# Kernel tuning notes

Measured on AMD Instinct MI355X. Metric: run time of the kernel, lower is better.

Reference implementation:

```python
import jax, jax.numpy as jnp
import numpy as np
import math

B, SQ, SK, HEADS, DH = 4, 4096, 308, 8, 64
INNER = HEADS * DH


def setup_inputs() -> dict:
    key = jax.random.key(0)
    k1, k2, k3, k4, k5 = jax.random.split(key, 5)
    q = jax.random.normal(k1, (B, SQ, INNER), dtype=jnp.float32)
    k = jax.random.normal(k2, (B, SK, INNER), dtype=jnp.float32)
    v = jax.random.normal(k3, (B, SK, INNER), dtype=jnp.float32)
    # mask_scale: positive multiplicative rescale (H*W / mask_area in original)
    mask_scale = jax.random.uniform(k4, (B, HEADS, SQ, SK), dtype=jnp.float32) + 0.5
    # mask_bool: region membership mask (masks > 0.5 in original)
    mask_bool = jax.random.randint(k5, (B, HEADS, SQ, SK), 0, 2) > 0
    return {"q": q, "k": k, "v": v, "mask_scale": mask_scale,
            "mask_bool": mask_bool, "heads": HEADS}


def reference(q, k, v, mask_scale, mask_bool, heads):
    b, sq, inner = q.shape
    dh = inner // heads
    # (b, s, h*dh) -> (b, h, s, dh)
    def split_heads(t):
        return t.reshape(b, -1, heads, dh).transpose(0, 2, 1, 3)
    qh, kh, vh = split_heads(q), split_heads(k), split_heads(v)
    scores = jnp.einsum('bhqd,bhkd->bhqk', qh, kh) / math.sqrt(dh)
    scores = scores * mask_scale
    scores = jnp.where(mask_bool, scores, -jnp.inf)
    attn = jax.nn.softmax(scores, axis=-1)
    out = jnp.einsum('bhqk,bhkd->bhqd', attn, vh)
    # (b, h, q, dh) -> (b, q, h*dh)
    return out.transpose(0, 2, 1, 3).reshape(b, sq, heads * dh)
```

## Files before the change

### kernel.cpp

```cpp
#include <hip/hip_runtime.h>


#define NB     4
#define NSQ    4096
#define NSK    308
#define NH     8
#define NDH    64
#define NINNER 512
#define NKT    20
#define QBLK   64
#define NTHREADS 256
#define NCH    (QBLK*NSK/4)

#define KFRAG_PER_BH (NKT*2*64*8)
#define VFRAG_PER_BH (NKT*4*64*4)
#define WS_BYTES ((size_t)(NB*NH) * (KFRAG_PER_BH + VFRAG_PER_BH) * 2)

#define MLDS_F16  (QBLK*NSK)
#define LDS_BYTES ((MLDS_F16 + KFRAG_PER_BH) * 2)

typedef _Float16 h8 __attribute__((ext_vector_type(8)));
typedef _Float16 h4 __attribute__((ext_vector_type(4)));
typedef float    f4 __attribute__((ext_vector_type(4)));
typedef int      i4 __attribute__((ext_vector_type(4)));

__global__ __launch_bounds__(512) void omost_prep(
    const float* __restrict__ Kg, const float* __restrict__ Vg,
    _Float16* __restrict__ ws)
{
  const int bh  = blockIdx.x;
  const int b   = bh >> 3;
  const int h   = bh & 7;
  const int tid = threadIdx.x;

  _Float16* Kfrag = ws + (size_t)bh * KFRAG_PER_BH;
  _Float16* Vfrag = ws + (size_t)(NB*NH) * KFRAG_PER_BH + (size_t)bh * VFRAG_PER_BH;

  const float* Kb = Kg + (size_t)b * NSK * NINNER + h * NDH;
  #pragma unroll
  for (int i = 0; i < (NKT*2*64) / 512; ++i) {
    int s   = tid + i * 512;
    int l   = s & 63;
    int dhc = (s >> 6) & 1;
    int kt  = s >> 7;
    int row = kt * 16 + (l & 15);
    int col = dhc * 32 + ((l >> 4) << 3);
    h8 hk;
    #pragma unroll
    for (int j = 0; j < 8; ++j) hk[j] = (_Float16)0.f;
    if (row < NSK) {
      const float* p = Kb + (size_t)row * NINNER + col;
      f4 a = *(const f4*)p;
      f4 c = *(const f4*)(p + 4);
      hk[0]=(_Float16)a[0]; hk[1]=(_Float16)a[1]; hk[2]=(_Float16)a[2]; hk[3]=(_Float16)a[3];
      hk[4]=(_Float16)c[0]; hk[5]=(_Float16)c[1]; hk[6]=(_Float16)c[2]; hk[7]=(_Float16)c[3];
    }
    *(h8*)(Kfrag + (size_t)s * 8) = hk;
  }

  const float* Vb = Vg + (size_t)b * NSK * NINNER + h * NDH;
  #pragma unroll
  for (int i = 0; i < (NKT*4*64) / 512; ++i) {
    int s    = tid + i * 512;
    int l    = s & 63;
    int nt   = (s >> 6) & 3;
    int kt   = s >> 8;
    int col  = nt * 16 + (l & 15);
    int row0 = kt * 16 + ((l >> 4) << 2);
    h4 hv;
    #pragma unroll
    for (int j = 0; j < 4; ++j) hv[j] = (_Float16)0.f;
    #pragma unroll
    for (int j = 0; j < 4; ++j) {
      int row = row0 + j;
      if (row < NSK) hv[j] = (_Float16)Vb[(size_t)row * NINNER + col];
    }
    *(h4*)(Vfrag + (size_t)s * 4) = hv;
  }
}

__global__ __launch_bounds__(NTHREADS) void omost_attn(
    const float* __restrict__ Qg, const float* __restrict__ MSg,
    const int*   __restrict__ MBg, const _Float16* __restrict__ ws,
    float* __restrict__ Og)
{
  extern __shared__ __align__(16) _Float16 smem[];
  _Float16* Mlds = smem;
  _Float16* Klds = smem + MLDS_F16;

  const int tid  = threadIdx.x;
  const int lane = tid & 63;
  const int wv   = tid >> 6;
  const int lg   = lane >> 4;
  const int lr   = lane & 15;

  const int wg = blockIdx.x;
  const int qt = wg & (NSQ / QBLK - 1);
  const int bh = wg >> 6;
  const int b  = bh >> 3;
  const int h  = bh & 7;

  const int q0   = qt * QBLK + wv * 16;
  const int qrow = q0 + lr;

  const h8* KfG = (const h8*)(ws + (size_t)bh * KFRAG_PER_BH);
  const h4* Vf  = (const h4*)(ws + (size_t)(NB*NH) * KFRAG_PER_BH + (size_t)bh * VFRAG_PER_BH);

  const float* Qb = Qg + ((size_t)b * NSQ + qrow) * NINNER + h * NDH;
  f4 qraw[4];
  qraw[0] = *(const f4*)(Qb + lg * 8);
  qraw[1] = *(const f4*)(Qb + lg * 8 + 4);
  qraw[2] = *(const f4*)(Qb + 32 + lg * 8);
  qraw[3] = *(const f4*)(Qb + 32 + lg * 8 + 4);

  const size_t mbase = ((size_t)bh * NSQ + qt * QBLK) * NSK;
  #pragma unroll
  for (int g = 0; g < 4; ++g) {
    f4 msr[5]; i4 mbr[5];
    #pragma unroll
    for (int j = 0; j < 5; ++j) {
      int cc  = tid + (g * 5 + j) * NTHREADS;
      int ccl = cc < NCH ? cc : NCH - 1;
      msr[j] = *(const f4*)(MSg + mbase + 4 * (size_t)ccl);
      mbr[j] = *(const i4*)(MBg + mbase + 4 * (size_t)ccl);
    }
    #pragma unroll
    for (int j = 0; j < 5; ++j) {
      int cc = tid + (g * 5 + j) * NTHREADS;
      if (cc < NCH) {
        h4 fm;
        #pragma unroll
        for (int r = 0; r < 4; ++r)
          fm[r] = (mbr[j][r] != 0) ? (_Float16)msr[j][r] : (_Float16)0.f;
        *(h4*)(&Mlds[4 * cc]) = fm;
      }
    }
  }

  #pragma unroll
  for (int i = 0; i < (KFRAG_PER_BH/8) / NTHREADS; ++i)
    ((h8*)Klds)[tid + i * NTHREADS] = KfG[tid + i * NTHREADS];
  __syncthreads();

  h8 qf0, qf1;
  {
    f4 a = qraw[0], c = qraw[1];
    qf0[0]=(_Float16)(a[0]*0.125f); qf0[1]=(_Float16)(a[1]*0.125f);
    qf0[2]=(_Float16)(a[2]*0.125f); qf0[3]=(_Float16)(a[3]*0.125f);
    qf0[4]=(_Float16)(c[0]*0.125f); qf0[5]=(_Float16)(c[1]*0.125f);
    qf0[6]=(_Float16)(c[2]*0.125f); qf0[7]=(_Float16)(c[3]*0.125f);
    a = qraw[2]; c = qraw[3];
    qf1[0]=(_Float16)(a[0]*0.125f); qf1[1]=(_Float16)(a[1]*0.125f);
    qf1[2]=(_Float16)(a[2]*0.125f); qf1[3]=(_Float16)(a[3]*0.125f);
    qf1[4]=(_Float16)(c[0]*0.125f); qf1[5]=(_Float16)(c[1]*0.125f);
    qf1[6]=(_Float16)(c[2]*0.125f); qf1[7]=(_Float16)(c[3]*0.125f);
  }

  const int mlrow = (wv * 16 + lr) * NSK;
  const h8* KfL = (const h8*)Klds;
  f4 acc0 = {0.f,0.f,0.f,0.f}, acc1 = {0.f,0.f,0.f,0.f};
  f4 acc2 = {0.f,0.f,0.f,0.f}, acc3 = {0.f,0.f,0.f,0.f};
  float ssum = 0.f;

#define MK_KBL(kt_) ((kt_) * 16 + lg * 4 > (NSK - 4) ? (NSK - 4) : (kt_) * 16 + lg * 4)

#define COMPUTE(kt_, v0_, v1_, v2_, v3_)                                         \
  do {                                                                           \
    const int kb_ = (kt_) * 16 + lg * 4;                                         \
    h8 k0_ = KfL[((kt_) * 2 + 0) * 64 + lane];                                   \
    h8 k1_ = KfL[((kt_) * 2 + 1) * 64 + lane];                                   \
    h4 m_  = *(const h4*)(&Mlds[mlrow + MK_KBL(kt_)]);                           \
    f4 c_ = {0.f, 0.f, 0.f, 0.f};                                                \
    c_ = __builtin_amdgcn_mfma_f32_16x16x32_f16(k0_, qf0, c_, 0, 0, 0);          \
    c_ = __builtin_amdgcn_mfma_f32_16x16x32_f16(k1_, qf1, c_, 0, 0, 0);          \
    h4 pa_;                                                                      \
    _Pragma("unroll")                                                            \
    for (int r = 0; r < 4; ++r) {                                                \
      float mf_ = (float)m_[r];                                                  \
      bool ok_ = (kb_ + r < NSK) && (mf_ != 0.f);                                \
      float p_ = ok_ ? __expf(__builtin_fmaf(c_[r], mf_, -4.f)) : 0.f;           \
      ssum += p_;                                                                \
      pa_[r] = (_Float16)p_;                                                     \
    }                                                                            \
    acc0 = __builtin_amdgcn_mfma_f32_16x16x16f16(pa_, (v0_), acc0, 0, 0, 0);     \
    acc1 = __builtin_amdgcn_mfma_f32_16x16x16f16(pa_, (v1_), acc1, 0, 0, 0);     \
    acc2 = __builtin_amdgcn_mfma_f32_16x16x16f16(pa_, (v2_), acc2, 0, 0, 0);     \
    acc3 = __builtin_amdgcn_mfma_f32_16x16x16f16(pa_, (v3_), acc3, 0, 0, 0);     \
  } while (0)

  h4 vA0 = Vf[0 * 64 + lane], vA1 = Vf[1 * 64 + lane];
  h4 vA2 = Vf[2 * 64 + lane], vA3 = Vf[3 * 64 + lane];
  h4 vB0, vB1, vB2, vB3;

  #pragma unroll
  for (int p = 0; p < NKT / 2; ++p) {
    const int ktB = 2 * p + 1;
    vB0 = Vf[(ktB * 4 + 0) * 64 + lane];
    vB1 = Vf[(ktB * 4 + 1) * 64 + lane];
    vB2 = Vf[(ktB * 4 + 2) * 64 + lane];
    vB3 = Vf[(ktB * 4 + 3) * 64 + lane];
    COMPUTE(2 * p, vA0, vA1, vA2, vA3);
    const int ktA = (2 * p + 2 < NKT) ? (2 * p + 2) : (NKT - 1);
    vA0 = Vf[(ktA * 4 + 0) * 64 + lane];
    vA1 = Vf[(ktA * 4 + 1) * 64 + lane];
    vA2 = Vf[(ktA * 4 + 2) * 64 + lane];
    vA3 = Vf[(ktA * 4 + 3) * 64 + lane];
    COMPUTE(2 * p + 1, vB0, vB1, vB2, vB3);
  }
#undef COMPUTE
#undef MK_KBL

  ssum += __shfl_xor(ssum, 16, 64);
  ssum += __shfl_xor(ssum, 32, 64);
  const float inv = 1.f / fmaxf(ssum, 1e-30f);

  float invr[4];
  #pragma unroll
  for (int r = 0; r < 4; ++r) invr[r] = __shfl(inv, lg * 4 + r, 64);

  float* Ob = Og + (size_t)b * NSQ * NINNER + h * NDH;
  f4 accs[4] = {acc0, acc1, acc2, acc3};
  #pragma unroll
  for (int nt = 0; nt < 4; ++nt) {
    #pragma unroll
    for (int r = 0; r < 4; ++r) {
      int qq = q0 + lg * 4 + r;
      Ob[(size_t)qq * NINNER + nt * 16 + lr] = accs[nt][r] * invr[r];
    }
  }
}

extern "C" void kernel_launch(void* const* d_in, const int* in_sizes, int n_in,
                              void* d_out, int out_size, void* d_ws, size_t ws_size,
                              hipStream_t stream) {
  const float* Qg  = (const float*)d_in[0];
  const float* Kg  = (const float*)d_in[1];
  const float* Vg  = (const float*)d_in[2];
  const float* MSg = (const float*)d_in[3];
  const int*   MBg = (const int*)d_in[4];
  float* Og = (float*)d_out;
  _Float16* ws = (_Float16*)d_ws;

  if (ws_size < WS_BYTES) return;

  static_assert(LDS_BYTES <= 160 * 1024, "exceeds gfx950 LDS");
  (void)hipFuncSetAttribute((const void*)omost_attn,
                            hipFuncAttributeMaxDynamicSharedMemorySize, LDS_BYTES);

  omost_prep<<<dim3(NB*NH), dim3(512), 0, stream>>>(Kg, Vg, ws);

  const int nwg = NB * NH * (NSQ / QBLK);
  omost_attn<<<dim3(nwg), dim3(NTHREADS), LDS_BYTES, stream>>>(Qg, MSg, MBg, ws, Og);
}
```

Measured before the change: 109.4 us.

## Warp-specialize attention kernel with double-buffered mask staging across query tiles

Restructures the attention kernel so each workgroup processes 8 consecutive 64-row query tiles. Two producer waves stream the fused mask/scale tile into a double-buffered LDS region while four consumer waves compute on the previous tile. This aims to overlap mask loading with MFMA compute and to load K fragments once per 512 rows. In exchange the grid shrinks to one workgroup per CU, LDS use rises, and only two waves issue the dominant mask loads, which may reduce memory-level parallelism.

```diff
diff --git a/kernel.cpp b/kernel.cpp
--- a/kernel.cpp
+++ b/kernel.cpp
@@ -8,16 +8,20 @@
 #define NDH    64
 #define NINNER 512
 #define NKT    20
-#define QBLK   64
-#define NTHREADS 256
-#define NCH    (QBLK*NSK/4)
+#define TROWS  64
+#define NTILES 8
+#define SUPER  (NTILES*TROWS)
+#define NTHREADS 384
+#define NPROD  128
+#define NCH    (TROWS*NSK/4)
+#define MTILE  (TROWS*NSK)
 
 #define KFRAG_PER_BH (NKT*2*64*8)
 #define VFRAG_PER_BH (NKT*4*64*4)
 #define WS_BYTES ((size_t)(NB*NH) * (KFRAG_PER_BH + VFRAG_PER_BH) * 2)
 
-#define MLDS_F16  (QBLK*NSK)
-#define LDS_BYTES ((MLDS_F16 + KFRAG_PER_BH) * 2)
+#define LDS_F16   (2*MTILE + KFRAG_PER_BH)
+#define LDS_BYTES (LDS_F16 * 2)
 
 typedef _Float16 h8 __attribute__((ext_vector_type(8)));
 typedef _Float16 h4 __attribute__((ext_vector_type(4)));
@@ -85,8 +89,9 @@
     float* __restrict__ Og)
 {
   extern __shared__ __align__(16) _Float16 smem[];
-  _Float16* Mlds = smem;
-  _Float16* Klds = smem + MLDS_F16;
+  _Float16* Mb0  = smem;
+  _Float16* Mb1  = smem + MTILE;
+  _Float16* Klds = smem + 2 * MTILE;
 
   const int tid  = threadIdx.x;
   const int lane = tid & 63;
@@ -94,82 +99,67 @@
   const int lg   = lane >> 4;
   const int lr   = lane & 15;
 
-  const int wg = blockIdx.x;
-  const int qt = wg & (NSQ / QBLK - 1);
-  const int bh = wg >> 6;
-  const int b  = bh >> 3;
-  const int h  = bh & 7;
-
-  const int q0   = qt * QBLK + wv * 16;
-  const int qrow = q0 + lr;
+  const int wg    = blockIdx.x;
+  const int sup   = wg & (NSQ / SUPER - 1);
+  const int bh    = wg >> 3;
+  const int b     = bh >> 3;
+  const int h     = bh & 7;
+  const int qbase = sup * SUPER;
 
   const h8* KfG = (const h8*)(ws + (size_t)bh * KFRAG_PER_BH);
   const h4* Vf  = (const h4*)(ws + (size_t)(NB*NH) * KFRAG_PER_BH + (size_t)bh * VFRAG_PER_BH);
 
-  const float* Qb = Qg + ((size_t)b * NSQ + qrow) * NINNER + h * NDH;
-  f4 qraw[4];
-  qraw[0] = *(const f4*)(Qb + lg * 8);
-  qraw[1] = *(const f4*)(Qb + lg * 8 + 4);
-  qraw[2] = *(const f4*)(Qb + 32 + lg * 8);
-  qraw[3] = *(const f4*)(Qb + 32 + lg * 8 + 4);
-
-  const size_t mbase = ((size_t)bh * NSQ + qt * QBLK) * NSK;
-  #pragma unroll
-  for (int g = 0; g < 4; ++g) {
-    f4 msr[5]; i4 mbr[5];
-    #pragma unroll
-    for (int j = 0; j < 5; ++j) {
-      int cc  = tid + (g * 5 + j) * NTHREADS;
-      int ccl = cc < NCH ? cc : NCH - 1;
-      msr[j] = *(const f4*)(MSg + mbase + 4 * (size_t)ccl);
-      mbr[j] = *(const i4*)(MBg + mbase + 4 * (size_t)ccl);
-    }
-    #pragma unroll
-    for (int j = 0; j < 5; ++j) {
-      int cc = tid + (g * 5 + j) * NTHREADS;
-      if (cc < NCH) {
-        h4 fm;
-        #pragma unroll
-        for (int r = 0; r < 4; ++r)
-          fm[r] = (mbr[j][r] != 0) ? (_Float16)msr[j][r] : (_Float16)0.f;
-        *(h4*)(&Mlds[4 * cc]) = fm;
-      }
-    }
-  }
-
-  #pragma unroll
-  for (int i = 0; i < (KFRAG_PER_BH/8) / NTHREADS; ++i)
-    ((h8*)Klds)[tid + i * NTHREADS] = KfG[tid + i * NTHREADS];
+#define STAGE(tt_, buf_)                                                        \
+  do {                                                                          \
+    const size_t mb_ = ((size_t)bh * NSQ + qbase + (size_t)(tt_) * TROWS) * NSK;\
+    _Pragma("unroll")                                                           \
+    for (int g_ = 0; g_ < 8; ++g_) {                                            \
+      f4 msr_[5]; i4 mbr_[5];                                                   \
+      _Pragma("unroll")                                                         \
+      for (int j_ = 0; j_ < 5; ++j_) {                                          \
+        int cc_  = tid + (g_ * 5 + j_) * NPROD;                                 \
+        int ccl_ = cc_ < NCH ? cc_ : NCH - 1;                                   \
+        msr_[j_] = *(const f4*)(MSg + mb_ + 4 * (size_t)ccl_);                  \
+        mbr_[j_] = *(const i4*)(MBg + mb_ + 4 * (size_t)ccl_);                  \
+      }                                                                         \
+      _Pragma("unroll")                                                         \
+      for (int j_ = 0; j_ < 5; ++j_) {                                          \
+        int cc_ = tid + (g_ * 5 + j_) * NPROD;                                  \
+        if (cc_ < NCH) {                                                        \
+          h4 fm_;                                                               \
+          _Pragma("unroll")                                                     \
+          for (int r_ = 0; r_ < 4; ++r_)                                        \
+            fm_[r_] = (mbr_[j_][r_] != 0) ? (_Float16)msr_[j_][r_]              \
+                                          : (_Float16)0.f;                      \
+          *(h4*)(&(buf_)[4 * cc_]) = fm_;                                       \
+        }                                                                       \
+      }                                                                         \
+    }                                                                           \
+  } while (0)
+
+  if (wv < 2) {
+    STAGE(0, Mb0);
+  } else {
+    const int ctid = tid - NPROD;
+    #pragma unroll
+    for (int i = 0; i < (KFRAG_PER_BH/8) / 256; ++i)
+      ((h8*)Klds)[ctid + i * 256] = KfG[ctid + i * 256];
+  }
   __syncthreads();
 
-  h8 qf0, qf1;
-  {
-    f4 a = qraw[0], c = qraw[1];
-    qf0[0]=(_Float16)(a[0]*0.125f); qf0[1]=(_Float16)(a[1]*0.125f);
-    qf0[2]=(_Float16)(a[2]*0.125f); qf0[3]=(_Float16)(a[3]*0.125f);
-    qf0[4]=(_Float16)(c[0]*0.125f); qf0[5]=(_Float16)(c[1]*0.125f);
-    qf0[6]=(_Float16)(c[2]*0.125f); qf0[7]=(_Float16)(c[3]*0.125f);
-    a = qraw[2]; c = qraw[3];
-    qf1[0]=(_Float16)(a[0]*0.125f); qf1[1]=(_Float16)(a[1]*0.125f);
-    qf1[2]=(_Float16)(a[2]*0.125f); qf1[3]=(_Float16)(a[3]*0.125f);
-    qf1[4]=(_Float16)(c[0]*0.125f); qf1[5]=(_Float16)(c[1]*0.125f);
-    qf1[6]=(_Float16)(c[2]*0.125f); qf1[7]=(_Float16)(c[3]*0.125f);
-  }
-
-  const int mlrow = (wv * 16 + lr) * NSK;
   const h8* KfL = (const h8*)Klds;
-  f4 acc0 = {0.f,0.f,0.f,0.f}, acc1 = {0.f,0.f,0.f,0.f};
-  f4 acc2 = {0.f,0.f,0.f,0.f}, acc3 = {0.f,0.f,0.f,0.f};
-  float ssum = 0.f;
+  const int cw  = wv - 2;
+  const int mlrow = (cw * 16 + lr) * NSK;
+  float* Ob = Og + (size_t)b * NSQ * NINNER + h * NDH;
 
 #define MK_KBL(kt_) ((kt_) * 16 + lg * 4 > (NSK - 4) ? (NSK - 4) : (kt_) * 16 + lg * 4)
 
-#define COMPUTE(kt_, v0_, v1_, v2_, v3_)                                         \
+#define COMPUTE(kt_, buf_, v0_, v1_, v2_, v3_)                                   \
   do {                                                                           \
     const int kb_ = (kt_) * 16 + lg * 4;                                         \
     h8 k0_ = KfL[((kt_) * 2 + 0) * 64 + lane];                                   \
     h8 k1_ = KfL[((kt_) * 2 + 1) * 64 + lane];                                   \
-    h4 m_  = *(const h4*)(&Mlds[mlrow + MK_KBL(kt_)]);                           \
+    h4 m_  = *(const h4*)(&(buf_)[mlrow + MK_KBL(kt_)]);                         \
     f4 c_ = {0.f, 0.f, 0.f, 0.f};                                                \
     c_ = __builtin_amdgcn_mfma_f32_16x16x32_f16(k0_, qf0, c_, 0, 0, 0);          \
     c_ = __builtin_amdgcn_mfma_f32_16x16x32_f16(k1_, qf1, c_, 0, 0, 0);          \
@@ -188,46 +178,76 @@
     acc3 = __builtin_amdgcn_mfma_f32_16x16x16f16(pa_, (v3_), acc3, 0, 0, 0);     \
   } while (0)
 
-  h4 vA0 = Vf[0 * 64 + lane], vA1 = Vf[1 * 64 + lane];
-  h4 vA2 = Vf[2 * 64 + lane], vA3 = Vf[3 * 64 + lane];
-  h4 vB0, vB1, vB2, vB3;
-
-  #pragma unroll
-  for (int p = 0; p < NKT / 2; ++p) {
-    const int ktB = 2 * p + 1;
-    vB0 = Vf[(ktB * 4 + 0) * 64 + lane];
-    vB1 = Vf[(ktB * 4 + 1) * 64 + lane];
-    vB2 = Vf[(ktB * 4 + 2) * 64 + lane];
-    vB3 = Vf[(ktB * 4 + 3) * 64 + lane];
-    COMPUTE(2 * p, vA0, vA1, vA2, vA3);
-    const int ktA = (2 * p + 2 < NKT) ? (2 * p + 2) : (NKT - 1);
-    vA0 = Vf[(ktA * 4 + 0) * 64 + lane];
-    vA1 = Vf[(ktA * 4 + 1) * 64 + lane];
-    vA2 = Vf[(ktA * 4 + 2) * 64 + lane];
-    vA3 = Vf[(ktA * 4 + 3) * 64 + lane];
-    COMPUTE(2 * p + 1, vB0, vB1, vB2, vB3);
+  #pragma unroll 1
+  for (int t = 0; t < NTILES; ++t) {
+    _Float16* bufc = (t & 1) ? Mb1 : Mb0;
+    _Float16* bufn = (t & 1) ? Mb0 : Mb1;
+
+    if (wv < 2) {
+      if (t < NTILES - 1) STAGE(t + 1, bufn);
+    } else {
+      const int qrow = qbase + t * TROWS + cw * 16 + lr;
+      const float* Qb = Qg + ((size_t)b * NSQ + qrow) * NINNER + h * NDH;
+      f4 qa = *(const f4*)(Qb + lg * 8);
+      f4 qb = *(const f4*)(Qb + lg * 8 + 4);
+      f4 qc = *(const f4*)(Qb + 32 + lg * 8);
+      f4 qd = *(const f4*)(Qb + 32 + lg * 8 + 4);
+      h8 qf0, qf1;
+      qf0[0]=(_Float16)(qa[0]*0.125f); qf0[1]=(_Float16)(qa[1]*0.125f);
+      qf0[2]=(_Float16)(qa[2]*0.125f); qf0[3]=(_Float16)(qa[3]*0.125f);
+      qf0[4]=(_Float16)(qb[0]*0.125f); qf0[5]=(_Float16)(qb[1]*0.125f);
+      qf0[6]=(_Float16)(qb[2]*0.125f); qf0[7]=(_Float16)(qb[3]*0.125f);
+      qf1[0]=(_Float16)(qc[0]*0.125f); qf1[1]=(_Float16)(qc[1]*0.125f);
+      qf1[2]=(_Float16)(qc[2]*0.125f); qf1[3]=(_Float16)(qc[3]*0.125f);
+      qf1[4]=(_Float16)(qd[0]*0.125f); qf1[5]=(_Float16)(qd[1]*0.125f);
+      qf1[6]=(_Float16)(qd[2]*0.125f); qf1[7]=(_Float16)(qd[3]*0.125f);
+
+      f4 acc0 = {0.f,0.f,0.f,0.f}, acc1 = {0.f,0.f,0.f,0.f};
+      f4 acc2 = {0.f,0.f,0.f,0.f}, acc3 = {0.f,0.f,0.f,0.f};
+      float ssum = 0.f;
+
+      h4 vA0 = Vf[0 * 64 + lane], vA1 = Vf[1 * 64 + lane];
+      h4 vA2 = Vf[2 * 64 + lane], vA3 = Vf[3 * 64 + lane];
+      h4 vB0, vB1, vB2, vB3;
+      #pragma unroll
+      for (int p = 0; p < NKT / 2; ++p) {
+        const int ktB = 2 * p + 1;
+        vB0 = Vf[(ktB * 4 + 0) * 64 + lane];
+        vB1 = Vf[(ktB * 4 + 1) * 64 + lane];
+        vB2 = Vf[(ktB * 4 + 2) * 64 + lane];
+        vB3 = Vf[(ktB * 4 + 3) * 64 + lane];
+        COMPUTE(2 * p, bufc, vA0, vA1, vA2, vA3);
+        const int ktA = (2 * p + 2 < NKT) ? (2 * p + 2) : (NKT - 1);
+        vA0 = Vf[(ktA * 4 + 0) * 64 + lane];
+        vA1 = Vf[(ktA * 4 + 1) * 64 + lane];
+        vA2 = Vf[(ktA * 4 + 2) * 64 + lane];
+        vA3 = Vf[(ktA * 4 + 3) * 64 + lane];
+        COMPUTE(2 * p + 1, bufc, vB0, vB1, vB2, vB3);
+      }
+
+      ssum += __shfl_xor(ssum, 16, 64);
+      ssum += __shfl_xor(ssum, 32, 64);
+      const float inv = 1.f / fmaxf(ssum, 1e-30f);
+      float invr[4];
+      #pragma unroll
+      for (int r = 0; r < 4; ++r) invr[r] = __shfl(inv, lg * 4 + r, 64);
+
+      const int q0t = qbase + t * TROWS + cw * 16;
+      f4 accs[4] = {acc0, acc1, acc2, acc3};
+      #pragma unroll
+      for (int nt = 0; nt < 4; ++nt) {
+        #pragma unroll
+        for (int r = 0; r < 4; ++r) {
+          int qq = q0t + lg * 4 + r;
+          Ob[(size_t)qq * NINNER + nt * 16 + lr] = accs[nt][r] * invr[r];
+        }
+      }
+    }
+    __syncthreads();
   }
 #undef COMPUTE
 #undef MK_KBL
-
-  ssum += __shfl_xor(ssum, 16, 64);
-  ssum += __shfl_xor(ssum, 32, 64);
-  const float inv = 1.f / fmaxf(ssum, 1e-30f);
-
-  float invr[4];
-  #pragma unroll
-  for (int r = 0; r < 4; ++r) invr[r] = __shfl(inv, lg * 4 + r, 64);
-
-  float* Ob = Og + (size_t)b * NSQ * NINNER + h * NDH;
-  f4 accs[4] = {acc0, acc1, acc2, acc3};
-  #pragma unroll
-  for (int nt = 0; nt < 4; ++nt) {
-    #pragma unroll
-    for (int r = 0; r < 4; ++r) {
-      int qq = q0 + lg * 4 + r;
-      Ob[(size_t)qq * NINNER + nt * 16 + lr] = accs[nt][r] * invr[r];
-    }
-  }
+#undef STAGE
 }
 
 extern "C" void kernel_launch(void* const* d_in, const int* in_sizes, int n_in,
@@ -249,6 +269,6 @@
 
   omost_prep<<<dim3(NB*NH), dim3(512), 0, stream>>>(Kg, Vg, ws);
 
-  const int nwg = NB * NH * (NSQ / QBLK);
+  const int nwg = NB * NH * (NSQ / SUPER);
   omost_attn<<<dim3(nwg), dim3(NTHREADS), LDS_BYTES, stream>>>(Qg, MSg, MBg, ws, Og);
 }
```

Result: slower. 312.9 us (+186.1%).
